# Optimization experiments

Hardware: AMD Instinct MI355X
Metric: run time of the kernel (lower is better)

Reference implementation:

```python
import jax, jax.numpy as jnp
import numpy as np
from jax import lax

H = 145; W = 145; BANDS = 200; D_MODEL = 128; NUM_CLASSES = 17
# Mamba2 defaults: expand=2, headdim=64, d_state=128, d_conv=4, ngroups=1
D_INNER = 256; NHEADS = 4; HEADDIM = 64; D_STATE = 128; D_CONV = 4
D_IN_PROJ = 2 * D_INNER + 2 * D_STATE + NHEADS  # 772
CONV_DIM = D_INNER + 2 * D_STATE                # 512


def _gelu(x):
    return jax.nn.gelu(x, approximate=False)


def _ln(x, g, b, eps=1e-5):
    m = jnp.mean(x, -1, keepdims=True)
    v = jnp.mean((x - m) ** 2, -1, keepdims=True)
    return (x - m) * lax.rsqrt(v + eps) * g + b


def _adaptive_pool_last(x, out):
    # PyTorch AdaptiveAvgPool semantics along the last axis via integral image
    L = x.shape[-1]
    i = np.arange(out)
    starts = (i * L) // out
    ends = -((-(i + 1) * L) // out)  # ceil((i+1)*L/out)
    cs = jnp.concatenate([jnp.zeros(x.shape[:-1] + (1,), x.dtype), jnp.cumsum(x, -1)], -1)
    return (cs[..., ends] - cs[..., starts]) / jnp.asarray(ends - starts, x.dtype)


def _mamba2(u, in_w, conv_w, conv_b, dt_bias, A_log, D, norm_w, out_w):
    # u: (L, D_MODEL). Faithful Mamba2 reference path (batch=1 squeezed).
    L = u.shape[0]
    zxbcdt = u @ in_w                      # (L, 772)
    z = zxbcdt[:, :D_INNER]                # (L, 256)
    xBC = zxbcdt[:, D_INNER:2 * D_INNER + 2 * D_STATE]  # (L, 512)
    dt = jax.nn.softplus(zxbcdt[:, -NHEADS:] + dt_bias)  # (L, 4)
    # causal depthwise conv1d, kernel D_CONV, then SiLU
    xp = jnp.pad(xBC, ((D_CONV - 1, 0), (0, 0)))
    xBC = sum(xp[k:k + L] * conv_w[:, k] for k in range(D_CONV)) + conv_b
    xBC = jax.nn.silu(xBC)
    xh = xBC[:, :D_INNER].reshape(L, NHEADS, HEADDIM)     # (L, h, p)
    Bm = xBC[:, D_INNER:D_INNER + D_STATE]                # (L, n)
    Cm = xBC[:, D_INNER + D_STATE:]                       # (L, n)
    A = -jnp.exp(A_log)                                   # (h,)

    def step(state, inp):
        dt_t, x_t, B_t, C_t = inp          # (h,), (h,p), (n,), (n,)
        dA = jnp.exp(dt_t * A)             # (h,)
        state = state * dA[:, None, None] + (dt_t[:, None] * x_t)[:, :, None] * B_t[None, None, :]
        y_t = jnp.einsum('hpn,n->hp', state, C_t)
        return state, y_t

    s0 = jnp.zeros((NHEADS, HEADDIM, D_STATE), u.dtype)
    _, y = lax.scan(step, s0, (dt, xh, Bm, Cm))           # y: (L, h, p)
    y = y + D[None, :, None] * xh
    y = y.reshape(L, D_INNER) * jax.nn.silu(z)            # gated
    y = y * lax.rsqrt(jnp.mean(y * y, -1, keepdims=True) + 1e-5) * norm_w  # RMSNormGated
    return y @ out_w                                      # (L, D_MODEL)


def _forward(x, ln_pre_g, ln_pre_b, fe_w1, fe_b1, fe_w2, fe_b2,
             cv_w1, cv_b1, cv_w2, cv_b2, mp_w, mp_b, mp_ln_g, mp_ln_b,
             m_in_w, m_conv_w, m_conv_b, m_dt_bias, m_A_log, m_D, m_norm_w, m_out_w,
             cls_ln_g, cls_ln_b, cls_w1, cls_b1, cls_w2, cls_b2, cls_w3, cls_b3):
    h, w, _ = x.shape
    xn = _ln(x, ln_pre_g, ln_pre_b)
    # MLP feature branch
    f = _gelu(xn @ fe_w1 + fe_b1)
    f = _gelu(f @ fe_w2 + fe_b2)                          # (h, w, 128)
    # conv branch
    c = jnp.transpose(xn, (2, 0, 1))[None]                # (1, bands, h, w)
    dn = ('NCHW', 'OIHW', 'NCHW')
    c = lax.conv_general_dilated(c, cv_w1, (1, 1), [(2, 2), (2, 2)], dimension_numbers=dn)
    c = _gelu(c + cv_b1[None, :, None, None])             # (1, 32, 147, 147)
    c = lax.conv_general_dilated(c, cv_w2, (1, 1), [(1, 1), (1, 1)], dimension_numbers=dn)
    c = _gelu(c + cv_b2[None, :, None, None])             # (1, 64, 147, 147)
    c = _adaptive_pool_last(c, W)                         # pool width -> 145
    c = _adaptive_pool_last(c.swapaxes(-1, -2), H).swapaxes(-1, -2)  # pool height
    conv_feat = jnp.transpose(c[0], (1, 2, 0))            # (145, 145, 64)
    comb = jnp.concatenate([f, conv_feat], -1).reshape(h * w, 192)
    p = _gelu(_ln(comb @ mp_w + mp_b, mp_ln_g, mp_ln_b))  # (L, d_model)
    m = _mamba2(p, m_in_w, m_conv_w, m_conv_b, m_dt_bias, m_A_log, m_D, m_norm_w, m_out_w)
    r = m.reshape(h, w, D_MODEL)
    o = _ln(r, cls_ln_g, cls_ln_b)
    o = _gelu(o @ cls_w1 + cls_b1)
    o = _gelu(o @ cls_w2 + cls_b2)
    return o @ cls_w3 + cls_b3                            # (h, w, num_classes)


def setup_inputs() -> dict:
    key = jax.random.key(0)
    ks = jax.random.split(key, 16)
    def n(k, shape, s=0.02):
        return jax.random.normal(k, shape, jnp.float32) * s
    return dict(
        x=jax.random.normal(ks[0], (H, W, BANDS), jnp.float32),
        ln_pre_g=jnp.ones((BANDS,), jnp.float32), ln_pre_b=jnp.zeros((BANDS,), jnp.float32),
        fe_w1=n(ks[1], (BANDS, 256)), fe_b1=jnp.zeros((256,), jnp.float32),
        fe_w2=n(ks[2], (256, 128)), fe_b2=jnp.zeros((128,), jnp.float32),
        cv_w1=n(ks[3], (32, BANDS, 3, 3)), cv_b1=jnp.zeros((32,), jnp.float32),
        cv_w2=n(ks[4], (64, 32, 3, 3)), cv_b2=jnp.zeros((64,), jnp.float32),
        mp_w=n(ks[5], (192, D_MODEL)), mp_b=jnp.zeros((D_MODEL,), jnp.float32),
        mp_ln_g=jnp.ones((D_MODEL,), jnp.float32), mp_ln_b=jnp.zeros((D_MODEL,), jnp.float32),
        m_in_w=n(ks[6], (D_MODEL, D_IN_PROJ)),
        m_conv_w=n(ks[7], (CONV_DIM, D_CONV), 0.2), m_conv_b=jnp.zeros((CONV_DIM,), jnp.float32),
        m_dt_bias=jnp.full((NHEADS,), -4.0, jnp.float32),
        m_A_log=jnp.log(jnp.linspace(1.0, 16.0, NHEADS)).astype(jnp.float32),
        m_D=jnp.ones((NHEADS,), jnp.float32),
        m_norm_w=jnp.ones((D_INNER,), jnp.float32),
        m_out_w=n(ks[8], (D_INNER, D_MODEL)),
        cls_ln_g=jnp.ones((D_MODEL,), jnp.float32), cls_ln_b=jnp.zeros((D_MODEL,), jnp.float32),
        cls_w1=n(ks[9], (D_MODEL, 128)), cls_b1=jnp.zeros((128,), jnp.float32),
        cls_w2=n(ks[10], (128, 64)), cls_b2=jnp.zeros((64,), jnp.float32),
        cls_w3=n(ks[11], (64, NUM_CLASSES)), cls_b3=jnp.zeros((NUM_CLASSES,), jnp.float32),
    )


def reference(x, ln_pre_g, ln_pre_b, fe_w1, fe_b1, fe_w2, fe_b2,
              cv_w1, cv_b1, cv_w2, cv_b2, mp_w, mp_b, mp_ln_g, mp_ln_b,
              m_in_w, m_conv_w, m_conv_b, m_dt_bias, m_A_log, m_D, m_norm_w, m_out_w,
              cls_ln_g, cls_ln_b, cls_w1, cls_b1, cls_w2, cls_b2, cls_w3, cls_b3):
    return _forward(x, ln_pre_g, ln_pre_b, fe_w1, fe_b1, fe_w2, fe_b2,
                    cv_w1, cv_b1, cv_w2, cv_b2, mp_w, mp_b, mp_ln_g, mp_ln_b,
                    m_in_w, m_conv_w, m_conv_b, m_dt_bias, m_A_log, m_D, m_norm_w, m_out_w,
                    cls_ln_g, cls_ln_b, cls_w1, cls_b1, cls_w2, cls_b2, cls_w3, cls_b3)
```

## Files before the change

kernel.cpp:

```cpp
#include <hip/hip_runtime.h>
#include <math.h>

#define HW 21025
#define Hdim 145
#define Wdim 145
#define NBANDS 200
#define CONVH 147
#define CONVHW 21609
#define QC 64
#define NCH 329
#define DTP 21056
#define SP 72
#define SSD_GRID 1344

typedef __attribute__((ext_vector_type(4))) float fv4;
typedef __attribute__((ext_vector_type(8))) short short8;

#define OFF_XN   ((size_t)0)
#define OFF_F1   ((size_t)4205000)
#define OFF_COMB ((size_t)9587400)
#define OFF_P    ((size_t)13624200)
#define OFF_ZX   ((size_t)16315400)
#define OFF_XBC  ((size_t)32546700)
#define OFF_S    ((size_t)43311500)
#define OFF_DT   ((size_t)54092172)
#define OFF_CT   ((size_t)54176396)
#define OFF_W    ((size_t)54177712)

__device__ __forceinline__ float gelu_f(float x){
    return 0.5f * x * (1.0f + erff(x * 0.70710678118654752440f));
}
__device__ __forceinline__ float silu_f(float x){
    return x / (1.0f + expf(-x));
}

__device__ __forceinline__ void bf16_split(float x, unsigned short& hs, unsigned short& ls){
    unsigned u = __float_as_uint(x);
    hs = (unsigned short)(u >> 16);
    float hif = __uint_as_float(u & 0xFFFF0000u);
    float lof = x - hif;
    ls = (unsigned short)(__float_as_uint(lof) >> 16);
}
__device__ __forceinline__ unsigned pack2(unsigned short a, unsigned short b){
    return (unsigned)a | ((unsigned)b << 16);
}
__device__ __forceinline__ unsigned packsplit(float x){
    unsigned short hs, ls;
    bf16_split(x, hs, ls);
    return ((unsigned)hs << 16) | (unsigned)ls;
}
__device__ __forceinline__ float unpackf(unsigned u){
    return __uint_as_float(u & 0xFFFF0000u) + __uint_as_float(u << 16);
}
__device__ __forceinline__ void split8g(const float* p, short8& h8, short8& l8){
    fv4 v0 = *reinterpret_cast<const fv4*>(p);
    fv4 v1 = *reinterpret_cast<const fv4*>(p + 4);
    unsigned short hs, ls;
    #pragma unroll
    for (int j = 0; j < 4; j++){
        bf16_split(v0[j], hs, ls); h8[j] = (short)hs; l8[j] = (short)ls;
        bf16_split(v1[j], hs, ls); h8[4 + j] = (short)hs; l8[4 + j] = (short)ls;
    }
}
__device__ __forceinline__ void unpack8(const unsigned* p, short8& h8, short8& l8){
    uint4 a = *reinterpret_cast<const uint4*>(p);
    uint4 b = *reinterpret_cast<const uint4*>(p + 4);
    unsigned v0 = a.x, v1 = a.y, v2 = a.z, v3 = a.w;
    unsigned v4 = b.x, v5 = b.y, v6 = b.z, v7 = b.w;
    h8[0]=(short)(v0>>16); l8[0]=(short)(v0&0xFFFFu);
    h8[1]=(short)(v1>>16); l8[1]=(short)(v1&0xFFFFu);
    h8[2]=(short)(v2>>16); l8[2]=(short)(v2&0xFFFFu);
    h8[3]=(short)(v3>>16); l8[3]=(short)(v3&0xFFFFu);
    h8[4]=(short)(v4>>16); l8[4]=(short)(v4&0xFFFFu);
    h8[5]=(short)(v5>>16); l8[5]=(short)(v5&0xFFFFu);
    h8[6]=(short)(v6>>16); l8[6]=(short)(v6&0xFFFFu);
    h8[7]=(short)(v7>>16); l8[7]=(short)(v7&0xFFFFu);
}

__device__ __forceinline__ bool gemm_decode(int bid, int NXB, int NYB, int& bx, int& by){
    int m = bid & 7;
    int r = bid >> 3;
    bx = r % NXB;
    by = (r / NXB) * 8 + m;
    return by < NYB;
}
__host__ __forceinline__ int gemm_grid(int NXB, int NYB){ return 8 * ((NYB + 7) / 8) * NXB; }

template<int ACT>
__global__ void ln_kernel(const float* __restrict__ in, const float* __restrict__ g,
                          const float* __restrict__ b, float* __restrict__ out, int D){
    int row = blockIdx.x, tid = threadIdx.x;
    const float* r = in + (size_t)row * D;
    float s = 0.f, s2 = 0.f;
    for (int i = tid; i < D; i += 256){ float v = r[i]; s += v; s2 += v*v; }
    __shared__ float r1[4], r2[4];
    #pragma unroll
    for (int o = 32; o > 0; o >>= 1){ s += __shfl_down(s, o); s2 += __shfl_down(s2, o); }
    if ((tid & 63) == 0){ r1[tid >> 6] = s; r2[tid >> 6] = s2; }
    __syncthreads();
    float S = r1[0] + r1[1] + r1[2] + r1[3];
    float S2 = r2[0] + r2[1] + r2[2] + r2[3];
    float mean = S / (float)D;
    float var = S2 / (float)D - mean * mean;
    float rs = rsqrtf(fmaxf(var, 0.f) + 1e-5f);
    float* o_ = out + (size_t)row * D;
    for (int i = tid; i < D; i += 256){
        float v = (r[i] - mean) * rs * g[i] + b[i];
        if (ACT == 1) v = gelu_f(v);
        o_[i] = v;
    }
}

template<int ACT, int MI>
__global__ __launch_bounds__(256) void gemm_mfma_w(const float* __restrict__ A, int lda,
                                                   const float* __restrict__ B, int ldb,
                                                   const float* __restrict__ bias,
                                                   const float* __restrict__ lng,
                                                   const float* __restrict__ lnb,
                                                   float* __restrict__ C, int ldc,
                                                   int M, int N, int K, int NXB, int NYB){
    const int SA = 40;
    const int BM = MI * 32;
    __shared__ __align__(16) unsigned short Ah[BM * SA], Al[BM * SA];
    __shared__ __align__(16) unsigned short Bh[128 * SA], Bl[128 * SA];
    __shared__ float rs1[2][BM], rs2_[2][BM];
    int bx, by;
    if (!gemm_decode(blockIdx.x, NXB, NYB, bx, by)) return;
    int tid = threadIdx.x;
    int lane = tid & 63, wid = tid >> 6;
    int wy = wid >> 1, wx = wid & 1;
    int bm = by * BM, bn = bx * 128;
    int l15 = lane & 15, g = lane >> 4;

    fv4 acc[MI][4];
    #pragma unroll
    for (int i = 0; i < MI; i++)
        #pragma unroll
        for (int j = 0; j < 4; j++) acc[i][j] = (fv4){0.f,0.f,0.f,0.f};

    int bcol = tid & 127;
    int bk16 = (tid >> 7) * 16;
    bool bcol_ok = (bn + bcol) < N;

    int nK = (K + 31) / 32;
    for (int ks = 0; ks < nK; ks++){
        int k0 = ks * 32;
        #pragma unroll
        for (int f = 0; f < MI; f++){
            int idx = tid * MI + f;
            int row = idx >> 3, qd = idx & 7;
            fv4 v = (fv4){0.f,0.f,0.f,0.f};
            if ((bm + row) < M && (k0 + qd * 4 + 4) <= K)
                v = *reinterpret_cast<const fv4*>(A + (size_t)(bm + row) * lda + k0 + qd * 4);
            unsigned short hs[4], ls[4];
            #pragma unroll
            for (int j = 0; j < 4; j++) bf16_split(v[j], hs[j], ls[j]);
            unsigned off = row * SA + qd * 4;
            *reinterpret_cast<uint2*>(&Ah[off]) = make_uint2(pack2(hs[0],hs[1]), pack2(hs[2],hs[3]));
            *reinterpret_cast<uint2*>(&Al[off]) = make_uint2(pack2(ls[0],ls[1]), pack2(ls[2],ls[3]));
        }
        {
            unsigned short hs[16], ls[16];
            #pragma unroll
            for (int j = 0; j < 16; j++){
                int kk = k0 + bk16 + j;
                float v = (bcol_ok && kk < K) ? B[(size_t)kk * ldb + bn + bcol] : 0.f;
                bf16_split(v, hs[j], ls[j]);
            }
            unsigned off = bcol * SA + bk16;
            *reinterpret_cast<uint4*>(&Bh[off]) = make_uint4(pack2(hs[0],hs[1]), pack2(hs[2],hs[3]),
                                                             pack2(hs[4],hs[5]), pack2(hs[6],hs[7]));
            *reinterpret_cast<uint4*>(&Bh[off + 8]) = make_uint4(pack2(hs[8],hs[9]), pack2(hs[10],hs[11]),
                                                                 pack2(hs[12],hs[13]), pack2(hs[14],hs[15]));
            *reinterpret_cast<uint4*>(&Bl[off]) = make_uint4(pack2(ls[0],ls[1]), pack2(ls[2],ls[3]),
                                                             pack2(ls[4],ls[5]), pack2(ls[6],ls[7]));
            *reinterpret_cast<uint4*>(&Bl[off + 8]) = make_uint4(pack2(ls[8],ls[9]), pack2(ls[10],ls[11]),
                                                                 pack2(ls[12],ls[13]), pack2(ls[14],ls[15]));
        }
        __syncthreads();
        short8 afh[MI], afl[MI], bfh[4], bfl[4];
        #pragma unroll
        for (int mi = 0; mi < MI; mi++){
            unsigned off = (wy * (MI * 16) + mi * 16 + l15) * SA + g * 8;
            afh[mi] = *reinterpret_cast<const short8*>(&Ah[off]);
            afl[mi] = *reinterpret_cast<const short8*>(&Al[off]);
        }
        #pragma unroll
        for (int ni = 0; ni < 4; ni++){
            unsigned off = (wx * 64 + ni * 16 + l15) * SA + g * 8;
            bfh[ni] = *reinterpret_cast<const short8*>(&Bh[off]);
            bfl[ni] = *reinterpret_cast<const short8*>(&Bl[off]);
        }
        #pragma unroll
        for (int mi = 0; mi < MI; mi++)
            #pragma unroll
            for (int ni = 0; ni < 4; ni++){
                acc[mi][ni] = __builtin_amdgcn_mfma_f32_16x16x32_bf16(afh[mi], bfh[ni], acc[mi][ni], 0, 0, 0);
                acc[mi][ni] = __builtin_amdgcn_mfma_f32_16x16x32_bf16(afh[mi], bfl[ni], acc[mi][ni], 0, 0, 0);
                acc[mi][ni] = __builtin_amdgcn_mfma_f32_16x16x32_bf16(afl[mi], bfh[ni], acc[mi][ni], 0, 0, 0);
            }
        __syncthreads();
    }
    float bv[4], lgv[4], lbv[4];
    #pragma unroll
    for (int ni = 0; ni < 4; ni++){
        int cc = bn + wx * 64 + ni * 16 + l15;
        bool ok = cc < N;
        bv[ni]  = (bias && ok) ? bias[cc] : 0.f;
        if (ACT >= 2){ lgv[ni] = ok ? lng[cc] : 1.f; lbv[ni] = ok ? lnb[cc] : 0.f; }
    }
    if (ACT >= 2){
        #pragma unroll
        for (int mi = 0; mi < MI; mi++)
            #pragma unroll
            for (int j = 0; j < 4; j++){
                float s = 0.f, s2 = 0.f;
                #pragma unroll
                for (int ni = 0; ni < 4; ni++){
                    float v = acc[mi][ni][j] + bv[ni];
                    s += v; s2 += v * v;
                }
                #pragma unroll
                for (int o = 1; o < 16; o <<= 1){
                    s += __shfl_xor(s, o); s2 += __shfl_xor(s2, o);
                }
                int row = wy * (MI * 16) + mi * 16 + g * 4 + j;
                if (l15 == 0){ rs1[wx][row] = s; rs2_[wx][row] = s2; }
            }
        __syncthreads();
        #pragma unroll
        for (int mi = 0; mi < MI; mi++)
            #pragma unroll
            for (int j = 0; j < 4; j++){
                int row = wy * (MI * 16) + mi * 16 + g * 4 + j;
                int rr = bm + row;
                if (rr >= M) continue;
                float S = rs1[0][row] + rs1[1][row];
                float S2 = rs2_[0][row] + rs2_[1][row];
                float mean = S / 128.f;
                float var = S2 / 128.f - mean * mean;
                float rsq = rsqrtf(fmaxf(var, 0.f) + 1e-5f);
                #pragma unroll
                for (int ni = 0; ni < 4; ni++){
                    int cc = bn + wx * 64 + ni * 16 + l15;
                    float v = acc[mi][ni][j] + bv[ni];
                    v = (v - mean) * rsq * lgv[ni] + lbv[ni];
                    if (ACT == 3) v = gelu_f(v);
                    C[(size_t)rr * ldc + cc] = v;
                }
            }
    } else {
        #pragma unroll
        for (int mi = 0; mi < MI; mi++)
            #pragma unroll
            for (int ni = 0; ni < 4; ni++){
                int cc = bn + wx * 64 + ni * 16 + l15;
                if (cc >= N) continue;
                #pragma unroll
                for (int j = 0; j < 4; j++){
                    int rr = bm + wy * (MI * 16) + mi * 16 + g * 4 + j;
                    if (rr >= M) continue;
                    float v = acc[mi][ni][j] + bv[ni];
                    if (ACT == 1) v = gelu_f(v);
                    C[(size_t)rr * ldc + cc] = v;
                }
            }
    }
}

template<int ACT>
__global__ __launch_bounds__(256) void gemm_mfma(const float* __restrict__ A, int lda,
                                                 const float* __restrict__ B,
                                                 const float* __restrict__ bias,
                                                 float* __restrict__ C, int ldc,
                                                 int M, int N, int K, int NXB, int NYB){
    const int SA = 40;
    __shared__ __align__(16) unsigned short Ah[128 * SA], Al[128 * SA];
    __shared__ __align__(16) unsigned short Bh[64 * SA],  Bl[64 * SA];
    int bx, by;
    if (!gemm_decode(blockIdx.x, NXB, NYB, bx, by)) return;
    int tid = threadIdx.x;
    int lane = tid & 63, wid = tid >> 6;
    int wy = wid >> 1, wx = wid & 1;
    int bm = by * 128, bn = bx * 64;
    int l15 = lane & 15, g = lane >> 4;

    fv4 acc[4][2];
    #pragma unroll
    for (int i = 0; i < 4; i++)
        #pragma unroll
        for (int j = 0; j < 2; j++) acc[i][j] = (fv4){0.f,0.f,0.f,0.f};

    int am = tid >> 1;
    int aq = (tid & 1) * 4;
    bool arow_ok = (bm + am) < M;
    int bn_t = tid & 63;
    int bk8 = (tid >> 6) * 8;
    bool bcol_ok = (bn + bn_t) < N;

    int nK = (K + 31) / 32;
    for (int ks = 0; ks < nK; ks++){
        int k0 = ks * 32;
        const float* Ap = A + (size_t)(bm + am) * lda + k0;
        #pragma unroll
        for (int f = 0; f < 4; f++){
            int kq = aq + f;
            fv4 v = (fv4){0.f,0.f,0.f,0.f};
            if (arow_ok && (k0 + kq * 4 + 4) <= K)
                v = *reinterpret_cast<const fv4*>(Ap + kq * 4);
            unsigned short hs[4], ls[4];
            #pragma unroll
            for (int j = 0; j < 4; j++) bf16_split(v[j], hs[j], ls[j]);
            unsigned off = am * SA + kq * 4;
            *reinterpret_cast<uint2*>(&Ah[off]) = make_uint2(pack2(hs[0],hs[1]), pack2(hs[2],hs[3]));
            *reinterpret_cast<uint2*>(&Al[off]) = make_uint2(pack2(ls[0],ls[1]), pack2(ls[2],ls[3]));
        }
        {
            unsigned short hs[8], ls[8];
            #pragma unroll
            for (int j = 0; j < 8; j++){
                int kk = k0 + bk8 + j;
                float v = (bcol_ok && kk < K) ? B[(size_t)kk * N + bn + bn_t] : 0.f;
                bf16_split(v, hs[j], ls[j]);
            }
            unsigned off = bn_t * SA + bk8;
            *reinterpret_cast<uint4*>(&Bh[off]) = make_uint4(pack2(hs[0],hs[1]), pack2(hs[2],hs[3]),
                                                             pack2(hs[4],hs[5]), pack2(hs[6],hs[7]));
            *reinterpret_cast<uint4*>(&Bl[off]) = make_uint4(pack2(ls[0],ls[1]), pack2(ls[2],ls[3]),
                                                             pack2(ls[4],ls[5]), pack2(ls[6],ls[7]));
        }
        __syncthreads();
        short8 afh[4], afl[4], bfh[2], bfl[2];
        #pragma unroll
        for (int mi = 0; mi < 4; mi++){
            unsigned off = (wy * 64 + mi * 16 + l15) * SA + g * 8;
            afh[mi] = *reinterpret_cast<const short8*>(&Ah[off]);
            afl[mi] = *reinterpret_cast<const short8*>(&Al[off]);
        }
        #pragma unroll
        for (int ni = 0; ni < 2; ni++){
            unsigned off = (wx * 32 + ni * 16 + l15) * SA + g * 8;
            bfh[ni] = *reinterpret_cast<const short8*>(&Bh[off]);
            bfl[ni] = *reinterpret_cast<const short8*>(&Bl[off]);
        }
        #pragma unroll
        for (int mi = 0; mi < 4; mi++)
            #pragma unroll
            for (int ni = 0; ni < 2; ni++){
                acc[mi][ni] = __builtin_amdgcn_mfma_f32_16x16x32_bf16(afh[mi], bfh[ni], acc[mi][ni], 0, 0, 0);
                acc[mi][ni] = __builtin_amdgcn_mfma_f32_16x16x32_bf16(afh[mi], bfl[ni], acc[mi][ni], 0, 0, 0);
                acc[mi][ni] = __builtin_amdgcn_mfma_f32_16x16x32_bf16(afl[mi], bfh[ni], acc[mi][ni], 0, 0, 0);
            }
        __syncthreads();
    }
    #pragma unroll
    for (int mi = 0; mi < 4; mi++){
        #pragma unroll
        for (int ni = 0; ni < 2; ni++){
            int cc = bn + wx * 32 + ni * 16 + l15;
            if (cc >= N) continue;
            float bv = bias ? bias[cc] : 0.f;
            #pragma unroll
            for (int j = 0; j < 4; j++){
                int rr = bm + wy * 64 + mi * 16 + g * 4 + j;
                if (rr >= M) continue;
                float v = acc[mi][ni][j] + bv;
                if (ACT == 1) v = gelu_f(v);
                C[(size_t)rr * ldc + cc] = v;
            }
        }
    }
}

__global__ __launch_bounds__(256) void dt_from_p(const float* __restrict__ p,
                                                 const float* __restrict__ w,
                                                 const float* __restrict__ dtb,
                                                 float* __restrict__ dtbT){
    __shared__ float wl[512];
    int tid = threadIdx.x;
    for (int i = tid; i < 512; i += 256){
        int k = i >> 2, h = i & 3;
        wl[i] = w[(size_t)k * 772 + 768 + h];
    }
    __syncthreads();
    int t = blockIdx.x * 64 + (tid >> 2);
    int h = tid & 3;
    if (t >= HW) return;
    const float* pr = p + (size_t)t * 128;
    float s = 0.f;
    for (int k = 0; k < 128; k += 4){
        fv4 v = *reinterpret_cast<const fv4*>(pr + k);
        s += v[0]*wl[k*4+h] + v[1]*wl[(k+1)*4+h] + v[2]*wl[(k+2)*4+h] + v[3]*wl[(k+3)*4+h];
    }
    s += dtb[h];
    dtbT[h * DTP + t] = (s > 20.f) ? s : log1pf(expf(s));
}

template<int IC, int OC, int NCHUNK>
__global__ void prep_w(const float* __restrict__ w, unsigned short* __restrict__ Wh,
                       unsigned short* __restrict__ Wl){
    const int KP = NCHUNK * 288;
    int idx = blockIdx.x * 256 + threadIdx.x;
    if (idx >= OC * KP) return;
    int o = idx / KP, k = idx % KP;
    int ch = k / 288, rest = k % 288, t = rest / 32, c = rest & 31;
    int ci = ch * 32 + c;
    float v = (ci < IC) ? w[((size_t)o * IC + ci) * 9 + t] : 0.f;
    unsigned short hs, ls;
    bf16_split(v, hs, ls);
    Wh[idx] = hs; Wl[idx] = ls;
}

template<int IC, int OC, int PAD, int NCHUNK, int NFRAG>
__global__ __launch_bounds__(256) void conv_mfma(const float* __restrict__ in,
                                                 int inH, int inW,
                                                 const unsigned short* __restrict__ Wh,
                                                 const unsigned short* __restrict__ Wl,
                                                 const float* __restrict__ bias,
                                                 float* __restrict__ out){
    const int KP = NCHUNK * 288;
    const int CST = 40;
    __shared__ __align__(16) unsigned short Xh[3 * 68 * CST], Xl[3 * 68 * CST];
    int y = blockIdx.y;
    int x0 = blockIdx.x * 64;
    int tid = threadIdx.x;
    int lane = tid & 63, wid = tid >> 6;
    int wy = wid >> 1, wx = wid & 1;
    int l15 = lane & 15, g = lane >> 4;

    fv4 acc[2][NFRAG];
    #pragma unroll
    for (int mi = 0; mi < 2; mi++)
        #pragma unroll
        for (int ni = 0; ni < NFRAG; ni++) acc[mi][ni] = (fv4){0.f,0.f,0.f,0.f};

    for (int ch = 0; ch < NCHUNK; ch++){
        int ci0 = ch * 32;
        if (ch > 0) __syncthreads();
        for (int e = tid; e < 3 * 68 * 8; e += 256){
            int qd = e & 7;
            int c  = (e >> 3) % 68;
            int r  = e / 544;
            int iy = y - PAD + r, ix = x0 - PAD + c;
            fv4 v = (fv4){0.f,0.f,0.f,0.f};
            if ((unsigned)iy < (unsigned)inH && (unsigned)ix < (unsigned)inW &&
                (ci0 + qd * 4 + 4) <= IC)
                v = *reinterpret_cast<const fv4*>(in + ((size_t)iy * inW + ix) * IC + ci0 + qd * 4);
            unsigned short hs[4], ls[4];
            #pragma unroll
            for (int j = 0; j < 4; j++) bf16_split(v[j], hs[j], ls[j]);
            unsigned off = (r * 68 + c) * CST + qd * 4;
            *reinterpret_cast<uint2*>(&Xh[off]) = make_uint2(pack2(hs[0],hs[1]), pack2(hs[2],hs[3]));
            *reinterpret_cast<uint2*>(&Xl[off]) = make_uint2(pack2(ls[0],ls[1]), pack2(ls[2],ls[3]));
        }
        __syncthreads();
        #pragma unroll
        for (int t = 0; t < 9; t++){
            int ky = t / 3, kx = t % 3;
            short8 ah[2], al[2], bh[NFRAG], bl[NFRAG];
            #pragma unroll
            for (int mi = 0; mi < 2; mi++){
                unsigned off = (ky * 68 + wy * 32 + mi * 16 + l15 + kx) * CST + g * 8;
                ah[mi] = *reinterpret_cast<const short8*>(&Xh[off]);
                al[mi] = *reinterpret_cast<const short8*>(&Xl[off]);
            }
            #pragma unroll
            for (int ni = 0; ni < NFRAG; ni++){
                int oc = wx * (16 * NFRAG) + ni * 16 + l15;
                size_t woff = (size_t)oc * KP + ch * 288 + t * 32 + g * 8;
                bh[ni] = *reinterpret_cast<const short8*>(&Wh[woff]);
                bl[ni] = *reinterpret_cast<const short8*>(&Wl[woff]);
            }
            #pragma unroll
            for (int mi = 0; mi < 2; mi++)
                #pragma unroll
                for (int ni = 0; ni < NFRAG; ni++){
                    acc[mi][ni] = __builtin_amdgcn_mfma_f32_16x16x32_bf16(ah[mi], bh[ni], acc[mi][ni], 0, 0, 0);
                    acc[mi][ni] = __builtin_amdgcn_mfma_f32_16x16x32_bf16(ah[mi], bl[ni], acc[mi][ni], 0, 0, 0);
                    acc[mi][ni] = __builtin_amdgcn_mfma_f32_16x16x32_bf16(al[mi], bh[ni], acc[mi][ni], 0, 0, 0);
                }
        }
    }
    #pragma unroll
    for (int mi = 0; mi < 2; mi++)
        #pragma unroll
        for (int ni = 0; ni < NFRAG; ni++){
            int oc = wx * (16 * NFRAG) + ni * 16 + l15;
            float bv = bias[oc];
            #pragma unroll
            for (int j = 0; j < 4; j++){
                int x = x0 + wy * 32 + mi * 16 + g * 4 + j;
                if (x >= CONVH) continue;
                out[((size_t)y * CONVH + x) * OC + oc] = gelu_f(acc[mi][ni][j] + bv);
            }
        }
}

__global__ void pool_kernel(const float* __restrict__ c2, float* __restrict__ comb){
    int idx = blockIdx.x * 256 + threadIdx.x;
    if (idx >= HW * 64) return;
    int o = idx & 63;
    int pix = idx >> 6;
    int xo = pix % Wdim, yo = pix / Wdim;
    int ys = yo * CONVH / Hdim, ye = ((yo + 1) * CONVH + Hdim - 1) / Hdim;
    int xs = xo * CONVH / Wdim, xe = ((xo + 1) * CONVH + Wdim - 1) / Wdim;
    float s = 0.f;
    for (int yy = ys; yy < ye; yy++)
        for (int xx = xs; xx < xe; xx++)
            s += c2[((size_t)yy * CONVH + xx) * 64 + o];
    comb[(size_t)pix * 192 + 128 + o] = s / (float)((ye - ys) * (xe - xs));
}

__global__ __launch_bounds__(256) void conv1d_tiled(const float* __restrict__ zx,
                                                    const float* __restrict__ w,
                                                    const float* __restrict__ b,
                                                    unsigned* __restrict__ xbcp){
    __shared__ float xs[67 * 128];
    __shared__ float wc[4 * 128];
    __shared__ float bc[128];
    int t0 = blockIdx.y * 64;
    int c0 = blockIdx.x * 128;
    int tid = threadIdx.x;
    for (int e = tid; e < 67 * 128; e += 256){
        int rr = e >> 7, cc = e & 127;
        int t = t0 - 3 + rr;
        xs[e] = (t >= 0 && t < HW) ? zx[(size_t)t * 772 + 256 + c0 + cc] : 0.f;
    }
    if (tid < 128){
        bc[tid] = b[c0 + tid];
        #pragma unroll
        for (int k = 0; k < 4; k++) wc[k * 128 + tid] = w[(c0 + tid) * 4 + k];
    }
    __syncthreads();
    for (int e = tid; e < 64 * 128; e += 256){
        int tt = e >> 7, cc = e & 127;
        if (t0 + tt >= HW) continue;
        float acc = bc[cc];
        #pragma unroll
        for (int k = 0; k < 4; k++) acc += xs[(tt + k) * 128 + cc] * wc[k * 128 + cc];
        xbcp[(size_t)(t0 + tt) * 512 + c0 + cc] = packsplit(silu_f(acc));
    }
}

__device__ __forceinline__ void chunk_cumsum_t(const float* __restrict__ dtbT, int t0, int Q,
                                               int h, const float* __restrict__ A_log,
                                               float* cum, float* dth){
    int tid = threadIdx.x;
    if (tid < 64){
        float d = (tid < Q) ? dtbT[h * DTP + t0 + tid] : 0.f;
        dth[tid] = d;
        float A = -expf(A_log[h]);
        float a = d * A;
        #pragma unroll
        for (int off = 1; off < 64; off <<= 1){
            float u = __shfl_up(a, off);
            if (tid >= off) a += u;
        }
        cum[tid] = a;
    }
    __syncthreads();
}

__device__ __forceinline__ bool ssd_decode(int bid, int& c, int& h){
    int m = bid & 7, rest = bid >> 3;
    h = rest & 3;
    c = (rest >> 2) * 8 + m;
    return c < NCH;
}

__global__ __launch_bounds__(256) void ssd_phaseA(const unsigned* __restrict__ xbcp,
                                                  const float* __restrict__ dtbT,
                                                  const float* __restrict__ A_log,
                                                  unsigned* __restrict__ Sp,
                                                  float* __restrict__ chunkT){
    __shared__ __align__(16) unsigned short BTh[128 * SP], BTl[128 * SP];
    __shared__ __align__(16) unsigned short XTh[64 * SP],  XTl[64 * SP];
    __shared__ float cum[64], dth[64], wln[64];
    int c, h;
    if (!ssd_decode(blockIdx.x, c, h)) return;
    int t0 = c * QC, Q = min(QC, HW - t0);
    int tid = threadIdx.x;
    chunk_cumsum_t(dtbT, t0, Q, h, A_log, cum, dth);
    float T = cum[Q - 1];
    if (tid == 0) chunkT[c * 4 + h] = T;
    if (tid < 64) wln[tid] = (tid < Q) ? __expf(T - cum[tid]) * dth[tid] : 0.f;
    __syncthreads();
    for (int e2 = tid; e2 < 4096; e2 += 256){
        int nn = e2 & 127, sp = e2 >> 7;
        int s0 = 2 * sp;
        unsigned v0 = (s0 < Q)     ? xbcp[(size_t)(t0 + s0) * 512 + 256 + nn] : 0u;
        unsigned v1 = (s0 + 1 < Q) ? xbcp[(size_t)(t0 + s0 + 1) * 512 + 256 + nn] : 0u;
        *reinterpret_cast<unsigned*>(&BTh[nn * SP + s0]) = pack2((unsigned short)(v0 >> 16), (unsigned short)(v1 >> 16));
        *reinterpret_cast<unsigned*>(&BTl[nn * SP + s0]) = pack2((unsigned short)(v0 & 0xFFFFu), (unsigned short)(v1 & 0xFFFFu));
    }
    for (int e2 = tid; e2 < 2048; e2 += 256){
        int pp = e2 & 63, sp = e2 >> 6;
        int s0 = 2 * sp;
        float v0 = (s0 < Q)     ? unpackf(xbcp[(size_t)(t0 + s0) * 512 + h * 64 + pp]) * wln[s0] : 0.f;
        float v1 = (s0 + 1 < Q) ? unpackf(xbcp[(size_t)(t0 + s0 + 1) * 512 + h * 64 + pp]) * wln[s0 + 1] : 0.f;
        unsigned short h0, l0, h1, l1;
        bf16_split(v0, h0, l0); bf16_split(v1, h1, l1);
        *reinterpret_cast<unsigned*>(&XTh[pp * SP + s0]) = pack2(h0, h1);
        *reinterpret_cast<unsigned*>(&XTl[pp * SP + s0]) = pack2(l0, l1);
    }
    __syncthreads();
    int lane = tid & 63, wid = tid >> 6;
    int wy = wid >> 1, wx = wid & 1;
    int l15 = lane & 15, g = lane >> 4;
    fv4 acc[2][4];
    #pragma unroll
    for (int mi = 0; mi < 2; mi++)
        #pragma unroll
        for (int ni = 0; ni < 4; ni++) acc[mi][ni] = (fv4){0.f,0.f,0.f,0.f};
    #pragma unroll
    for (int ks = 0; ks < 2; ks++){
        short8 ah[2], al[2], bh_[4], bl_[4];
        #pragma unroll
        for (int mi = 0; mi < 2; mi++){
            unsigned off = (wy * 32 + mi * 16 + l15) * SP + ks * 32 + g * 8;
            ah[mi] = *reinterpret_cast<const short8*>(&XTh[off]);
            al[mi] = *reinterpret_cast<const short8*>(&XTl[off]);
        }
        #pragma unroll
        for (int ni = 0; ni < 4; ni++){
            unsigned off = (wx * 64 + ni * 16 + l15) * SP + ks * 32 + g * 8;
            bh_[ni] = *reinterpret_cast<const short8*>(&BTh[off]);
            bl_[ni] = *reinterpret_cast<const short8*>(&BTl[off]);
        }
        #pragma unroll
        for (int mi = 0; mi < 2; mi++)
            #pragma unroll
            for (int ni = 0; ni < 4; ni++){
                acc[mi][ni] = __builtin_amdgcn_mfma_f32_16x16x32_bf16(ah[mi], bh_[ni], acc[mi][ni], 0, 0, 0);
                acc[mi][ni] = __builtin_amdgcn_mfma_f32_16x16x32_bf16(ah[mi], bl_[ni], acc[mi][ni], 0, 0, 0);
                acc[mi][ni] = __builtin_amdgcn_mfma_f32_16x16x32_bf16(al[mi], bh_[ni], acc[mi][ni], 0, 0, 0);
            }
    }
    size_t sb = (size_t)(c * 4 + h) * 8192;
    #pragma unroll
    for (int mi = 0; mi < 2; mi++)
        #pragma unroll
        for (int ni = 0; ni < 4; ni++)
            #pragma unroll
            for (int j = 0; j < 4; j++){
                int p = wy * 32 + mi * 16 + g * 4 + j;
                int n = wx * 64 + ni * 16 + l15;
                Sp[sb + p * 128 + n] = packsplit(acc[mi][ni][j]);
            }
}

__global__ __launch_bounds__(256) void ssd_phaseB(unsigned* __restrict__ Sp,
                                                  const float* __restrict__ chunkT){
    __shared__ float e[NCH];
    int tid = threadIdx.x;
    int idx = blockIdx.x * 256 + tid;
    int h = idx >> 13, pn = idx & 8191;
    for (int c = tid; c < NCH; c += 256) e[c] = __expf(chunkT[c * 4 + h]);
    __syncthreads();
    #define ADDR_(cc) Sp[((size_t)((cc) * 4 + h)) * 8192 + pn]
    unsigned r0 = ADDR_(0), r1 = ADDR_(1), r2 = ADDR_(2), r3 = ADDR_(3);
    float s = 0.f;
    int c = 0;
    for (; c + 8 <= NCH; c += 4){
        unsigned n0 = ADDR_(c + 4), n1 = ADDR_(c + 5), n2 = ADDR_(c + 6), n3 = ADDR_(c + 7);
        ADDR_(c) = packsplit(s);     s = fmaf(s, e[c],     unpackf(r0));
        ADDR_(c + 1) = packsplit(s); s = fmaf(s, e[c + 1], unpackf(r1));
        ADDR_(c + 2) = packsplit(s); s = fmaf(s, e[c + 2], unpackf(r2));
        ADDR_(c + 3) = packsplit(s); s = fmaf(s, e[c + 3], unpackf(r3));
        r0 = n0; r1 = n1; r2 = n2; r3 = n3;
    }
    for (; c < NCH; c++){
        unsigned nx = (c + 4 < NCH) ? ADDR_(c + 4) : 0u;
        float loc = unpackf(r0); r0 = r1; r1 = r2; r2 = r3; r3 = nx;
        ADDR_(c) = packsplit(s);
        s = fmaf(s, e[c], loc);
    }
    #undef ADDR_
}

__global__ __launch_bounds__(256) void ssd_phaseC(const unsigned* __restrict__ xbcp,
                                                  const float* __restrict__ dtbT,
                                                  const float* __restrict__ A_log,
                                                  const float* __restrict__ Dvec,
                                                  const unsigned* __restrict__ Sp,
                                                  float* __restrict__ y){
    __shared__ __align__(16) unsigned short U0h[64 * SP], U0l[64 * SP];
    __shared__ __align__(16) unsigned short U1h[64 * SP], U1l[64 * SP];
    __shared__ float cum[64], dth[64];
    int c, h;
    if (!ssd_decode(blockIdx.x, c, h)) return;
    int t0 = c * QC, Q = min(QC, HW - t0);
    int tid = threadIdx.x;
    chunk_cumsum_t(dtbT, t0, Q, h, A_log, cum, dth);
    int lane = tid & 63, wid = tid >> 6;
    int wy = wid >> 1, wx = wid & 1;
    int l15 = lane & 15, g = lane >> 4;

    int trow[2], srow[2], prow[2];
    #pragma unroll
    for (int i = 0; i < 2; i++){
        trow[i] = min(t0 + wy * 32 + i * 16 + l15, HW - 1);
        srow[i] = min(t0 + wx * 32 + i * 16 + l15, HW - 1);
        prow[i] = wx * 32 + i * 16 + l15;
    }

    fv4 accG[2][2], accA[2][2];
    #pragma unroll
    for (int mi = 0; mi < 2; mi++)
        #pragma unroll
        for (int ni = 0; ni < 2; ni++){ accG[mi][ni] = (fv4){0.f,0.f,0.f,0.f}; accA[mi][ni] = (fv4){0.f,0.f,0.f,0.f}; }

    const unsigned* Sbase = Sp + (size_t)(c * 4 + h) * 8192;
    #pragma unroll
    for (int k0 = 0; k0 < 128; k0 += 32){
        short8 ah[2], al[2], bh[2], bl[2], sh[2], sl[2];
        #pragma unroll
        for (int mi = 0; mi < 2; mi++)
            unpack8(xbcp + (size_t)trow[mi] * 512 + 384 + k0 + g * 8, ah[mi], al[mi]);
        #pragma unroll
        for (int ni = 0; ni < 2; ni++){
            unpack8(xbcp + (size_t)srow[ni] * 512 + 256 + k0 + g * 8, bh[ni], bl[ni]);
            unpack8(Sbase + prow[ni] * 128 + k0 + g * 8, sh[ni], sl[ni]);
        }
        #pragma unroll
        for (int mi = 0; mi < 2; mi++)
            #pragma unroll
            for (int ni = 0; ni < 2; ni++){
                accG[mi][ni] = __builtin_amdgcn_mfma_f32_16x16x32_bf16(ah[mi], bh[ni], accG[mi][ni], 0, 0, 0);
                accG[mi][ni] = __builtin_amdgcn_mfma_f32_16x16x32_bf16(ah[mi], bl[ni], accG[mi][ni], 0, 0, 0);
                accG[mi][ni] = __builtin_amdgcn_mfma_f32_16x16x32_bf16(al[mi], bh[ni], accG[mi][ni], 0, 0, 0);
                accA[mi][ni] = __builtin_amdgcn_mfma_f32_16x16x32_bf16(ah[mi], sh[ni], accA[mi][ni], 0, 0, 0);
                accA[mi][ni] = __builtin_amdgcn_mfma_f32_16x16x32_bf16(ah[mi], sl[ni], accA[mi][ni], 0, 0, 0);
                accA[mi][ni] = __builtin_amdgcn_mfma_f32_16x16x32_bf16(al[mi], sh[ni], accA[mi][ni], 0, 0, 0);
            }
    }
    #pragma unroll
    for (int mi = 0; mi < 2; mi++)
        #pragma unroll
        for (int ni = 0; ni < 2; ni++)
            #pragma unroll
            for (int j = 0; j < 4; j++){
                int t = wy * 32 + mi * 16 + g * 4 + j;
                int s = wx * 32 + ni * 16 + l15;
                float pv = 0.f;
                if (s <= t && s < Q)
                    pv = accG[mi][ni][j] * __expf(cum[t] - cum[s]) * dth[s];
                unsigned short hs, ls;
                bf16_split(pv, hs, ls);
                U0h[t * SP + s] = hs;
                U0l[t * SP + s] = ls;
            }
    for (int e2 = tid; e2 < 2048; e2 += 256){
        int pp = e2 & 63, sp = e2 >> 6;
        int s0 = 2 * sp;
        unsigned v0 = (s0 < Q)     ? xbcp[(size_t)(t0 + s0) * 512 + h * 64 + pp] : 0u;
        unsigned v1 = (s0 + 1 < Q) ? xbcp[(size_t)(t0 + s0 + 1) * 512 + h * 64 + pp] : 0u;
        *reinterpret_cast<unsigned*>(&U1h[pp * SP + s0]) = pack2((unsigned short)(v0 >> 16), (unsigned short)(v1 >> 16));
        *reinterpret_cast<unsigned*>(&U1l[pp * SP + s0]) = pack2((unsigned short)(v0 & 0xFFFFu), (unsigned short)(v1 & 0xFFFFu));
    }
    __syncthreads();
    fv4 accY[2][2];
    #pragma unroll
    for (int mi = 0; mi < 2; mi++)
        #pragma unroll
        for (int ni = 0; ni < 2; ni++)
            #pragma unroll
            for (int j = 0; j < 4; j++){
                int t = wy * 32 + mi * 16 + g * 4 + j;
                accY[mi][ni][j] = __expf(cum[t]) * accA[mi][ni][j];
            }
    #pragma unroll
    for (int kk = 0; kk < 2; kk++){
        short8 ph[2], pl[2], xh[2], xl[2];
        #pragma unroll
        for (int mi = 0; mi < 2; mi++){
            unsigned off = (wy * 32 + mi * 16 + l15) * SP + kk * 32 + g * 8;
            ph[mi] = *reinterpret_cast<const short8*>(&U0h[off]);
            pl[mi] = *reinterpret_cast<const short8*>(&U0l[off]);
        }
        #pragma unroll
        for (int ni = 0; ni < 2; ni++){
            unsigned off = (wx * 32 + ni * 16 + l15) * SP + kk * 32 + g * 8;
            xh[ni] = *reinterpret_cast<const short8*>(&U1h[off]);
            xl[ni] = *reinterpret_cast<const short8*>(&U1l[off]);
        }
        #pragma unroll
        for (int mi = 0; mi < 2; mi++)
            #pragma unroll
            for (int ni = 0; ni < 2; ni++){
                accY[mi][ni] = __builtin_amdgcn_mfma_f32_16x16x32_bf16(ph[mi], xh[ni], accY[mi][ni], 0, 0, 0);
                accY[mi][ni] = __builtin_amdgcn_mfma_f32_16x16x32_bf16(ph[mi], xl[ni], accY[mi][ni], 0, 0, 0);
                accY[mi][ni] = __builtin_amdgcn_mfma_f32_16x16x32_bf16(pl[mi], xh[ni], accY[mi][ni], 0, 0, 0);
            }
    }
    float Dh = Dvec[h];
    #pragma unroll
    for (int mi = 0; mi < 2; mi++)
        #pragma unroll
        for (int ni = 0; ni < 2; ni++)
            #pragma unroll
            for (int j = 0; j < 4; j++){
                int t = wy * 32 + mi * 16 + g * 4 + j;
                if (t >= Q) continue;
                int p = wx * 32 + ni * 16 + l15;
                float xv = unpackf(xbcp[(size_t)(t0 + t) * 512 + h * 64 + p]);
                y[(size_t)(t0 + t) * 256 + h * 64 + p] = accY[mi][ni][j] + Dh * xv;
            }
}

__global__ void gated_rms_kernel(float* __restrict__ y, const float* __restrict__ zx,
                                 const float* __restrict__ nw){
    int row = blockIdx.x, tid = threadIdx.x;
    float v = y[(size_t)row * 256 + tid];
    float z = zx[(size_t)row * 772 + tid];
    v *= silu_f(z);
    float s = v * v;
    __shared__ float r1[4];
    #pragma unroll
    for (int o = 32; o > 0; o >>= 1) s += __shfl_down(s, o);
    if ((tid & 63) == 0) r1[tid >> 6] = s;
    __syncthreads();
    float S = r1[0] + r1[1] + r1[2] + r1[3];
    float rs = rsqrtf(S / 256.f + 1e-5f);
    y[(size_t)row * 256 + tid] = v * rs * nw[tid];
}

extern "C" void kernel_launch(void* const* d_in, const int* in_sizes, int n_in,
                              void* d_out, int out_size, void* d_ws, size_t ws_size,
                              hipStream_t stream){
    (void)in_sizes; (void)n_in; (void)out_size; (void)ws_size;
    const float* x        = (const float*)d_in[0];
    const float* ln_pre_g = (const float*)d_in[1];
    const float* ln_pre_b = (const float*)d_in[2];
    const float* fe_w1    = (const float*)d_in[3];
    const float* fe_b1    = (const float*)d_in[4];
    const float* fe_w2    = (const float*)d_in[5];
    const float* fe_b2    = (const float*)d_in[6];
    const float* cv_w1    = (const float*)d_in[7];
    const float* cv_b1    = (const float*)d_in[8];
    const float* cv_w2    = (const float*)d_in[9];
    const float* cv_b2    = (const float*)d_in[10];
    const float* mp_w     = (const float*)d_in[11];
    const float* mp_b     = (const float*)d_in[12];
    const float* mp_ln_g  = (const float*)d_in[13];
    const float* mp_ln_b  = (const float*)d_in[14];
    const float* m_in_w   = (const float*)d_in[15];
    const float* m_conv_w = (const float*)d_in[16];
    const float* m_conv_b = (const float*)d_in[17];
    const float* m_dtb    = (const float*)d_in[18];
    const float* m_A_log  = (const float*)d_in[19];
    const float* m_D      = (const float*)d_in[20];
    const float* m_norm_w = (const float*)d_in[21];
    const float* m_out_w  = (const float*)d_in[22];
    const float* cls_ln_g = (const float*)d_in[23];
    const float* cls_ln_b = (const float*)d_in[24];
    const float* cls_w1   = (const float*)d_in[25];
    const float* cls_b1   = (const float*)d_in[26];
    const float* cls_w2   = (const float*)d_in[27];
    const float* cls_b2   = (const float*)d_in[28];
    const float* cls_w3   = (const float*)d_in[29];
    const float* cls_b3   = (const float*)d_in[30];

    float* ws   = (float*)d_ws;
    float* xn   = ws + OFF_XN;
    float* f1   = ws + OFF_F1;
    float* comb = ws + OFF_COMB;
    float* p    = ws + OFF_P;
    float* zx   = ws + OFF_ZX;
    unsigned* xbcp = (unsigned*)(ws + OFF_XBC);
    unsigned* Sp = (unsigned*)(ws + OFF_S);
    float* dtbT = ws + OFF_DT;
    float* chkT = ws + OFF_CT;
    float* c1h  = ws + OFF_XBC;
    float* c2h  = ws + OFF_XBC + 691488;
    float* ybuf = ws + OFF_F1;
    float* cls0 = ws + OFF_XN;
    float* cls1 = ws + OFF_P;
    float* cls2 = ws + OFF_COMB + 2691200;
    unsigned short* W1h = (unsigned short*)(ws + OFF_W);
    unsigned short* W1l = (unsigned short*)(ws + OFF_W + 32256);
    unsigned short* W2h = (unsigned short*)(ws + OFF_W + 64512);
    unsigned short* W2l = (unsigned short*)(ws + OFF_W + 73728);

    prep_w<200, 32, 7><<<(32 * 2016 + 255) / 256, 256, 0, stream>>>(cv_w1, W1h, W1l);
    prep_w<32, 64, 1><<<(64 * 288 + 255) / 256, 256, 0, stream>>>(cv_w2, W2h, W2l);
    ln_kernel<0><<<HW, 256, 0, stream>>>(x, ln_pre_g, ln_pre_b, xn, NBANDS);
    gemm_mfma_w<1, 4><<<gemm_grid(2, 165), 256, 0, stream>>>(xn, 200, fe_w1, 256, fe_b1,
        (const float*)nullptr, (const float*)nullptr, f1, 256, HW, 256, 200, 2, 165);
    gemm_mfma_w<1, 2><<<gemm_grid(1, 329), 256, 0, stream>>>(f1, 256, fe_w2, 128, fe_b2,
        (const float*)nullptr, (const float*)nullptr, comb, 192, HW, 128, 256, 1, 329);
    conv_mfma<200, 32, 2, 7, 1><<<dim3(3, CONVH), 256, 0, stream>>>(xn, Hdim, Wdim, W1h, W1l, cv_b1, c1h);
    conv_mfma<32, 64, 1, 1, 2><<<dim3(3, CONVH), 256, 0, stream>>>(c1h, CONVH, CONVH, W2h, W2l, cv_b2, c2h);
    pool_kernel<<<(HW * 64 + 255) / 256, 256, 0, stream>>>(c2h, comb);
    gemm_mfma_w<3, 2><<<gemm_grid(1, 329), 256, 0, stream>>>(comb, 192, mp_w, 128, mp_b,
        mp_ln_g, mp_ln_b, p, 128, HW, 128, 192, 1, 329);
    gemm_mfma_w<0, 4><<<gemm_grid(6, 165), 256, 0, stream>>>(p, 128, m_in_w, 772,
        (const float*)nullptr, (const float*)nullptr, (const float*)nullptr,
        zx, 772, HW, 768, 128, 6, 165);
    dt_from_p<<<(HW + 63) / 64, 256, 0, stream>>>(p, m_in_w, m_dtb, dtbT);
    conv1d_tiled<<<dim3(4, NCH), 256, 0, stream>>>(zx, m_conv_w, m_conv_b, xbcp);
    ssd_phaseA<<<SSD_GRID, 256, 0, stream>>>(xbcp, dtbT, m_A_log, Sp, chkT);
    ssd_phaseB<<<128, 256, 0, stream>>>(Sp, chkT);
    ssd_phaseC<<<SSD_GRID, 256, 0, stream>>>(xbcp, dtbT, m_A_log, m_D, Sp, ybuf);
    gated_rms_kernel<<<HW, 256, 0, stream>>>(ybuf, zx, m_norm_w);
    gemm_mfma_w<2, 2><<<gemm_grid(1, 329), 256, 0, stream>>>(ybuf, 256, m_out_w, 128,
        (const float*)nullptr, cls_ln_g, cls_ln_b, cls0, 128, HW, 128, 256, 1, 329);
    gemm_mfma_w<1, 2><<<gemm_grid(1, 329), 256, 0, stream>>>(cls0, 128, cls_w1, 128, cls_b1,
        (const float*)nullptr, (const float*)nullptr, cls1, 128, HW, 128, 128, 1, 329);
    gemm_mfma<1><<<gemm_grid(1, 165), 256, 0, stream>>>(cls1, 128, cls_w2, cls_b2, cls2, 64, HW, 64, 128, 1, 165);
    gemm_mfma<0><<<gemm_grid(1, 165), 256, 0, stream>>>(cls2, 64, cls_w3, cls_b3, (float*)d_out, 17, HW, 17, 64, 1, 165);
}
```

Baseline: 474.9 us.

## Store inter-chunk SSD states as single bf16 and fuse gate into phaseC

Switches the chunk state buffer from a packed hi/lo bf16 split (32-bit) to a single rounded bf16 (16-bit), halving its traffic in phases A, B and C and dropping one MFMA per state product. The intra-chunk decay matrix in phaseC is also kept as a single bf16, dropping its lo part and one MFMA. The SiLU(z) gating moves from the RMS kernel into phaseC's epilogue. This trades accuracy, since the lower-order correction terms are lost on a long recurrence, for less memory bandwidth and compute.

```diff
diff --git a/kernel.cpp b/kernel.cpp
--- a/kernel.cpp
+++ b/kernel.cpp
@@ -52,15 +52,13 @@
 __device__ __forceinline__ float unpackf(unsigned u){
     return __uint_as_float(u & 0xFFFF0000u) + __uint_as_float(u << 16);
 }
-__device__ __forceinline__ void split8g(const float* p, short8& h8, short8& l8){
-    fv4 v0 = *reinterpret_cast<const fv4*>(p);
-    fv4 v1 = *reinterpret_cast<const fv4*>(p + 4);
-    unsigned short hs, ls;
-    #pragma unroll
-    for (int j = 0; j < 4; j++){
-        bf16_split(v0[j], hs, ls); h8[j] = (short)hs; l8[j] = (short)ls;
-        bf16_split(v1[j], hs, ls); h8[4 + j] = (short)hs; l8[4 + j] = (short)ls;
-    }
+__device__ __forceinline__ unsigned short bf16rnd(float x){
+    unsigned u = __float_as_uint(x);
+    unsigned r = u + 0x7FFFu + ((u >> 16) & 1u);
+    return (unsigned short)(r >> 16);
+}
+__device__ __forceinline__ float bf16f(unsigned short h){
+    return __uint_as_float((unsigned)h << 16);
 }
 __device__ __forceinline__ void unpack8(const unsigned* p, short8& h8, short8& l8){
     uint4 a = *reinterpret_cast<const uint4*>(p);
@@ -571,7 +569,7 @@
 __global__ __launch_bounds__(256) void ssd_phaseA(const unsigned* __restrict__ xbcp,
                                                   const float* __restrict__ dtbT,
                                                   const float* __restrict__ A_log,
-                                                  unsigned* __restrict__ Sp,
+                                                  unsigned short* __restrict__ Sb,
                                                   float* __restrict__ chunkT){
     __shared__ __align__(16) unsigned short BTh[128 * SP], BTl[128 * SP];
     __shared__ __align__(16) unsigned short XTh[64 * SP],  XTl[64 * SP];
@@ -645,11 +643,11 @@
             for (int j = 0; j < 4; j++){
                 int p = wy * 32 + mi * 16 + g * 4 + j;
                 int n = wx * 64 + ni * 16 + l15;
-                Sp[sb + p * 128 + n] = packsplit(acc[mi][ni][j]);
-            }
-}
-
-__global__ __launch_bounds__(256) void ssd_phaseB(unsigned* __restrict__ Sp,
+                Sb[sb + p * 128 + n] = bf16rnd(acc[mi][ni][j]);
+            }
+}
+
+__global__ __launch_bounds__(256) void ssd_phaseB(unsigned short* __restrict__ Sb,
                                                   const float* __restrict__ chunkT){
     __shared__ float e[NCH];
     int tid = threadIdx.x;
@@ -657,34 +655,35 @@
     int h = idx >> 13, pn = idx & 8191;
     for (int c = tid; c < NCH; c += 256) e[c] = __expf(chunkT[c * 4 + h]);
     __syncthreads();
-    #define ADDR_(cc) Sp[((size_t)((cc) * 4 + h)) * 8192 + pn]
-    unsigned r0 = ADDR_(0), r1 = ADDR_(1), r2 = ADDR_(2), r3 = ADDR_(3);
+    #define ADDR_(cc) Sb[((size_t)((cc) * 4 + h)) * 8192 + pn]
+    unsigned short r0 = ADDR_(0), r1 = ADDR_(1), r2 = ADDR_(2), r3 = ADDR_(3);
     float s = 0.f;
     int c = 0;
     for (; c + 8 <= NCH; c += 4){
-        unsigned n0 = ADDR_(c + 4), n1 = ADDR_(c + 5), n2 = ADDR_(c + 6), n3 = ADDR_(c + 7);
-        ADDR_(c) = packsplit(s);     s = fmaf(s, e[c],     unpackf(r0));
-        ADDR_(c + 1) = packsplit(s); s = fmaf(s, e[c + 1], unpackf(r1));
-        ADDR_(c + 2) = packsplit(s); s = fmaf(s, e[c + 2], unpackf(r2));
-        ADDR_(c + 3) = packsplit(s); s = fmaf(s, e[c + 3], unpackf(r3));
+        unsigned short n0 = ADDR_(c + 4), n1 = ADDR_(c + 5), n2 = ADDR_(c + 6), n3 = ADDR_(c + 7);
+        ADDR_(c) = bf16rnd(s);     s = fmaf(s, e[c],     bf16f(r0));
+        ADDR_(c + 1) = bf16rnd(s); s = fmaf(s, e[c + 1], bf16f(r1));
+        ADDR_(c + 2) = bf16rnd(s); s = fmaf(s, e[c + 2], bf16f(r2));
+        ADDR_(c + 3) = bf16rnd(s); s = fmaf(s, e[c + 3], bf16f(r3));
         r0 = n0; r1 = n1; r2 = n2; r3 = n3;
     }
     for (; c < NCH; c++){
-        unsigned nx = (c + 4 < NCH) ? ADDR_(c + 4) : 0u;
-        float loc = unpackf(r0); r0 = r1; r1 = r2; r2 = r3; r3 = nx;
-        ADDR_(c) = packsplit(s);
+        unsigned short nx = (c + 4 < NCH) ? ADDR_(c + 4) : (unsigned short)0;
+        float loc = bf16f(r0); r0 = r1; r1 = r2; r2 = r3; r3 = nx;
+        ADDR_(c) = bf16rnd(s);
         s = fmaf(s, e[c], loc);
     }
     #undef ADDR_
 }
 
 __global__ __launch_bounds__(256) void ssd_phaseC(const unsigned* __restrict__ xbcp,
+                                                  const float* __restrict__ zx,
                                                   const float* __restrict__ dtbT,
                                                   const float* __restrict__ A_log,
                                                   const float* __restrict__ Dvec,
-                                                  const unsigned* __restrict__ Sp,
+                                                  const unsigned short* __restrict__ Sb,
                                                   float* __restrict__ y){
-    __shared__ __align__(16) unsigned short U0h[64 * SP], U0l[64 * SP];
+    __shared__ __align__(16) unsigned short U0[64 * SP];
     __shared__ __align__(16) unsigned short U1h[64 * SP], U1l[64 * SP];
     __shared__ float cum[64], dth[64];
     int c, h;
@@ -710,17 +709,17 @@
         #pragma unroll
         for (int ni = 0; ni < 2; ni++){ accG[mi][ni] = (fv4){0.f,0.f,0.f,0.f}; accA[mi][ni] = (fv4){0.f,0.f,0.f,0.f}; }
 
-    const unsigned* Sbase = Sp + (size_t)(c * 4 + h) * 8192;
+    const unsigned short* Sbase = Sb + (size_t)(c * 4 + h) * 8192;
     #pragma unroll
     for (int k0 = 0; k0 < 128; k0 += 32){
-        short8 ah[2], al[2], bh[2], bl[2], sh[2], sl[2];
+        short8 ah[2], al[2], bh[2], bl[2], sh[2];
         #pragma unroll
         for (int mi = 0; mi < 2; mi++)
             unpack8(xbcp + (size_t)trow[mi] * 512 + 384 + k0 + g * 8, ah[mi], al[mi]);
         #pragma unroll
         for (int ni = 0; ni < 2; ni++){
             unpack8(xbcp + (size_t)srow[ni] * 512 + 256 + k0 + g * 8, bh[ni], bl[ni]);
-            unpack8(Sbase + prow[ni] * 128 + k0 + g * 8, sh[ni], sl[ni]);
+            sh[ni] = *reinterpret_cast<const short8*>(Sbase + prow[ni] * 128 + k0 + g * 8);
         }
         #pragma unroll
         for (int mi = 0; mi < 2; mi++)
@@ -730,7 +729,6 @@
                 accG[mi][ni] = __builtin_amdgcn_mfma_f32_16x16x32_bf16(ah[mi], bl[ni], accG[mi][ni], 0, 0, 0);
                 accG[mi][ni] = __builtin_amdgcn_mfma_f32_16x16x32_bf16(al[mi], bh[ni], accG[mi][ni], 0, 0, 0);
                 accA[mi][ni] = __builtin_amdgcn_mfma_f32_16x16x32_bf16(ah[mi], sh[ni], accA[mi][ni], 0, 0, 0);
-                accA[mi][ni] = __builtin_amdgcn_mfma_f32_16x16x32_bf16(ah[mi], sl[ni], accA[mi][ni], 0, 0, 0);
                 accA[mi][ni] = __builtin_amdgcn_mfma_f32_16x16x32_bf16(al[mi], sh[ni], accA[mi][ni], 0, 0, 0);
             }
     }
@@ -745,10 +743,7 @@
                 float pv = 0.f;
                 if (s <= t && s < Q)
                     pv = accG[mi][ni][j] * __expf(cum[t] - cum[s]) * dth[s];
-                unsigned short hs, ls;
-                bf16_split(pv, hs, ls);
-                U0h[t * SP + s] = hs;
-                U0l[t * SP + s] = ls;
+                U0[t * SP + s] = bf16rnd(pv);
             }
     for (int e2 = tid; e2 < 2048; e2 += 256){
         int pp = e2 & 63, sp = e2 >> 6;
@@ -771,12 +766,11 @@
             }
     #pragma unroll
     for (int kk = 0; kk < 2; kk++){
-        short8 ph[2], pl[2], xh[2], xl[2];
+        short8 ph[2], xh[2], xl[2];
         #pragma unroll
         for (int mi = 0; mi < 2; mi++){
             unsigned off = (wy * 32 + mi * 16 + l15) * SP + kk * 32 + g * 8;
-            ph[mi] = *reinterpret_cast<const short8*>(&U0h[off]);
-            pl[mi] = *reinterpret_cast<const short8*>(&U0l[off]);
+            ph[mi] = *reinterpret_cast<const short8*>(&U0[off]);
         }
         #pragma unroll
         for (int ni = 0; ni < 2; ni++){
@@ -790,7 +784,6 @@
             for (int ni = 0; ni < 2; ni++){
                 accY[mi][ni] = __builtin_amdgcn_mfma_f32_16x16x32_bf16(ph[mi], xh[ni], accY[mi][ni], 0, 0, 0);
                 accY[mi][ni] = __builtin_amdgcn_mfma_f32_16x16x32_bf16(ph[mi], xl[ni], accY[mi][ni], 0, 0, 0);
-                accY[mi][ni] = __builtin_amdgcn_mfma_f32_16x16x32_bf16(pl[mi], xh[ni], accY[mi][ni], 0, 0, 0);
             }
     }
     float Dh = Dvec[h];
@@ -804,16 +797,14 @@
                 if (t >= Q) continue;
                 int p = wx * 32 + ni * 16 + l15;
                 float xv = unpackf(xbcp[(size_t)(t0 + t) * 512 + h * 64 + p]);
-                y[(size_t)(t0 + t) * 256 + h * 64 + p] = accY[mi][ni][j] + Dh * xv;
-            }
-}
-
-__global__ void gated_rms_kernel(float* __restrict__ y, const float* __restrict__ zx,
-                                 const float* __restrict__ nw){
+                float zv = zx[(size_t)(t0 + t) * 772 + h * 64 + p];
+                y[(size_t)(t0 + t) * 256 + h * 64 + p] = (accY[mi][ni][j] + Dh * xv) * silu_f(zv);
+            }
+}
+
+__global__ void rms_kernel(float* __restrict__ y, const float* __restrict__ nw){
     int row = blockIdx.x, tid = threadIdx.x;
     float v = y[(size_t)row * 256 + tid];
-    float z = zx[(size_t)row * 772 + tid];
-    v *= silu_f(z);
     float s = v * v;
     __shared__ float r1[4];
     #pragma unroll
@@ -868,7 +859,7 @@
     float* p    = ws + OFF_P;
     float* zx   = ws + OFF_ZX;
     unsigned* xbcp = (unsigned*)(ws + OFF_XBC);
-    unsigned* Sp = (unsigned*)(ws + OFF_S);
+    unsigned short* Sb = (unsigned short*)(ws + OFF_S);
     float* dtbT = ws + OFF_DT;
     float* chkT = ws + OFF_CT;
     float* c1h  = ws + OFF_XBC;
@@ -899,10 +890,10 @@
         zx, 772, HW, 768, 128, 6, 165);
     dt_from_p<<<(HW + 63) / 64, 256, 0, stream>>>(p, m_in_w, m_dtb, dtbT);
     conv1d_tiled<<<dim3(4, NCH), 256, 0, stream>>>(zx, m_conv_w, m_conv_b, xbcp);
-    ssd_phaseA<<<SSD_GRID, 256, 0, stream>>>(xbcp, dtbT, m_A_log, Sp, chkT);
-    ssd_phaseB<<<128, 256, 0, stream>>>(Sp, chkT);
-    ssd_phaseC<<<SSD_GRID, 256, 0, stream>>>(xbcp, dtbT, m_A_log, m_D, Sp, ybuf);
-    gated_rms_kernel<<<HW, 256, 0, stream>>>(ybuf, zx, m_norm_w);
+    ssd_phaseA<<<SSD_GRID, 256, 0, stream>>>(xbcp, dtbT, m_A_log, Sb, chkT);
+    ssd_phaseB<<<128, 256, 0, stream>>>(Sb, chkT);
+    ssd_phaseC<<<SSD_GRID, 256, 0, stream>>>(xbcp, zx, dtbT, m_A_log, m_D, Sb, ybuf);
+    rms_kernel<<<HW, 256, 0, stream>>>(ybuf, m_norm_w);
     gemm_mfma_w<2, 2><<<gemm_grid(1, 329), 256, 0, stream>>>(ybuf, 256, m_out_w, 128,
         (const float*)nullptr, cls_ln_g, cls_ln_b, cls0, 128, HW, 128, 256, 1, 329);
     gemm_mfma_w<1, 2><<<gemm_grid(1, 329), 256, 0, stream>>>(cls0, 128, cls_w1, 128, cls_b1,
```

New measurement: 469.3 us. No clear change (-1.2%).
